# Kernel tuning notes

Measured on AMD Instinct MI355X. Metric: run time of the kernel, lower is better.

Reference implementation:

```python
import jax, jax.numpy as jnp
import numpy as np

B, T, H, NH, DH, R = 2, 2048, 1024, 16, 64, 256
ALPHA = 0.6


def setup_inputs() -> dict:
    key = jax.random.key(0)
    ks = jax.random.split(key, 28)
    f32 = jnp.float32

    def nrm(k, shape, s=0.02):
        return jax.random.normal(k, shape, dtype=f32) * s

    inp = {}
    inp['x'] = jax.random.normal(ks[0], (B, T, H), dtype=f32)
    # additive causal mask [1,1,T,T]: 0 on/below diagonal, -1e9 above
    causal = jnp.tril(jnp.ones((T, T), dtype=bool))
    inp['attention_mask'] = jnp.where(causal, 0.0, -1e9).astype(f32)[None, None]
    # low-rank SVD factors for q,k,v,o: Vh [H,R], S [R] (positive), U [H,R], b [H]
    i = 1
    for name in ('q', 'k', 'v', 'o'):
        inp['Vh_' + name] = nrm(ks[i], (H, R)); i += 1
        inp['S_' + name] = jax.random.uniform(ks[i], (R,), dtype=f32, minval=0.5, maxval=1.5); i += 1
        inp['U_' + name] = nrm(ks[i], (H, R)); i += 1
        inp['b_' + name] = jnp.zeros((H,), dtype=f32); i += 1
    # full-rank weights of the original (fallback) attention: y = x @ W + b (Conv1D style)
    for name in ('q', 'k', 'v', 'o'):
        inp['W_' + name] = nrm(ks[i], (H, H)); i += 1
        inp['bf_' + name] = jnp.zeros((H,), dtype=f32); i += 1
    return inp


def _split_heads(t):
    # [B,T,H] -> [B,nH,T,dH]
    Bs, Ts, _ = t.shape
    return t.reshape(Bs, Ts, NH, DH).transpose(0, 2, 1, 3)


def _attention(Q, K, V, mask):
    q, k, v = _split_heads(Q), _split_heads(K), _split_heads(V)
    scores = jnp.einsum('bhtd,bhsd->bhts', q, k) / (DH ** 0.5)
    scores = scores + mask
    w = jax.nn.softmax(scores, axis=-1)
    ctx = jnp.einsum('bhts,bhsd->bhtd', w, v)
    Bs = ctx.shape[0]
    return ctx.transpose(0, 2, 1, 3).reshape(Bs, -1, NH * DH)


def _lowrank(x, Vh, S, U, b):
    # ((x @ Vh) * S) @ U.T + b
    return ((x @ Vh) * S) @ U.T + b


def reference(x, attention_mask,
              Vh_q, S_q, U_q, b_q, Vh_k, S_k, U_k, b_k,
              Vh_v, S_v, U_v, b_v, Vh_o, S_o, U_o, b_o,
              W_q, bf_q, W_k, bf_k, W_v, bf_v, W_o, bf_o):
    # --- low-rank SVD path ---
    Q = _lowrank(x, Vh_q, S_q, U_q, b_q)
    K = _lowrank(x, Vh_k, S_k, U_k, b_k)
    V = _lowrank(x, Vh_v, S_v, U_v, b_v)
    ctx = _attention(Q, K, V, attention_mask)
    out = _lowrank(ctx, Vh_o, S_o, U_o, b_o)
    # --- fallback: original full-rank attention ---
    Qf = x @ W_q + bf_q
    Kf = x @ W_k + bf_k
    Vf = x @ W_v + bf_v
    ctxf = _attention(Qf, Kf, Vf, attention_mask)
    fallback_out = ctxf @ W_o + bf_o
    return ALPHA * out + (1.0 - ALPHA) * fallback_out
```

## Files before the change

### kernel.cpp

```cpp
#include <hip/hip_runtime.h>
#include <hip/hip_bf16.h>

typedef __bf16 bf16_t;
typedef __bf16 bf16x4 __attribute__((ext_vector_type(4)));
typedef __bf16 bf16x8 __attribute__((ext_vector_type(8)));
typedef float f32x4 __attribute__((ext_vector_type(4)));
typedef _Float16 f16_t;
typedef _Float16 f16x4 __attribute__((ext_vector_type(4)));
typedef unsigned short us4 __attribute__((ext_vector_type(4)));

extern "C" __device__ float __ocml_native_exp2_f32(float);

#define DEVI static __device__ __forceinline__

static constexpr int TN   = 2048;
static constexpr int Hn   = 1024;
static constexpr int Rn   = 256;
static constexpr int MTOK = 4096;
static constexpr int NCAT = 6144;

static constexpr float QSCALE = 0.125f;
static constexpr float LOG2E  = 1.44269504088896340736f;
static constexpr float SOFT_OFF2 = 0.426950408889634f;

template <typename T>
DEVI void gload16(const T* g, T* l) {
    __builtin_amdgcn_global_load_lds(
        (const __attribute__((address_space(1))) void*)g,
        (__attribute__((address_space(3))) void*)l, 16, 0, 0);
}

DEVI float loadf(const void* base, int idx, bool bfm) {
    if (bfm) {
        unsigned int u = ((const unsigned short*)base)[idx];
        u <<= 16;
        return __builtin_bit_cast(float, u);
    }
    return ((const float*)base)[idx];
}
DEVI float4 loadf4(const void* base, int idx, bool bfm) {
    float4 f;
    if (bfm) {
        us4 u = *(const us4*)((const unsigned short*)base + idx);
        f.x = __builtin_bit_cast(float, (unsigned)u.x << 16);
        f.y = __builtin_bit_cast(float, (unsigned)u.y << 16);
        f.z = __builtin_bit_cast(float, (unsigned)u.z << 16);
        f.w = __builtin_bit_cast(float, (unsigned)u.w << 16);
    } else {
        f = *(const float4*)((const float*)base + idx);
    }
    return f;
}
DEVI bool detect_bf16(const void* mask) {
    return fabsf(((const float*)mask)[0]) > 1.0f;
}

struct PrepArgs {
    const void *x, *mask;
    const void *Vh[4], *S[4], *U[4];
    const void *bb[4], *bfb[4];
    const void *W[4];
    bf16_t *wdst[4];
    int wldd[4];
    float wscale[4];
    bf16_t *Xb, *Abuf, *Bbuf, *Ubuf, *VhTs;
    float *biascat, *biaso;
};

__global__ __launch_bounds__(256)
void k_prep(PrepArgs a) {
    const bool bfm = detect_bf16(a.mask);
    const int bid = blockIdx.x;
    const int tid = threadIdx.x;
    __shared__ float t[32][33];
    if (bid < 1024) {
        int i = (bid * 256 + tid) * 16;
#pragma unroll
        for (int j = 0; j < 4; ++j) {
            float4 f = loadf4(a.x, i + j * 4, bfm);
            bf16x4 o;
            o[0] = (bf16_t)f.x; o[1] = (bf16_t)f.y; o[2] = (bf16_t)f.z; o[3] = (bf16_t)f.w;
            *(bf16x4*)&a.Xb[i + j * 4] = o;
        }
    } else if (bid < 1280) {
        int e4 = ((bid - 1024) * 256 + tid) * 4;
        int r = e4 & 255;
        float4 s4 = loadf4(a.S[3], r, bfm);
        float4 u4 = loadf4(a.U[3], e4, bfm);
        float4 v4 = loadf4(a.Vh[3], e4, bfm);
        bf16x4 ao, bo;
        ao[0] = (bf16_t)(u4.x * s4.x * 0.6f); ao[1] = (bf16_t)(u4.y * s4.y * 0.6f);
        ao[2] = (bf16_t)(u4.z * s4.z * 0.6f); ao[3] = (bf16_t)(u4.w * s4.w * 0.6f);
        bo[0] = (bf16_t)v4.x; bo[1] = (bf16_t)v4.y; bo[2] = (bf16_t)v4.z; bo[3] = (bf16_t)v4.w;
        *(bf16x4*)&a.Abuf[e4] = ao;
        *(bf16x4*)&a.Bbuf[e4] = bo;
    } else if (bid < 1472) {
        int i = ((bid - 1280) * 256 + tid) * 16;
        int proj = i >> 18;
        int e = i & 262143;
#pragma unroll
        for (int j = 0; j < 4; ++j) {
            float4 f = loadf4(a.U[proj], e + j * 4, bfm);
            bf16x4 o;
            o[0] = (bf16_t)f.x; o[1] = (bf16_t)f.y; o[2] = (bf16_t)f.z; o[3] = (bf16_t)f.w;
            *(bf16x4*)&a.Ubuf[i + j * 4] = o;
        }
    } else if (bid < 2240) {
        const int tb = bid - 1472;
        const int proj = tb >> 8;
        const int rem = tb & 255;
        const int bx = (rem & 7) * 32;
        const int by = (rem >> 3) * 32;
        const int tx = tid & 31, ty = tid >> 5;
        const float sc = (proj == 0) ? QSCALE * LOG2E : 1.0f;
        bf16_t* dst = a.VhTs + (size_t)proj * Rn * Hn;
#pragma unroll
        for (int k = 0; k < 32; k += 8)
            t[ty + k][tx] = loadf(a.Vh[proj], (by + ty + k) * Rn + bx + tx, bfm);
        __syncthreads();
#pragma unroll
        for (int k = 0; k < 32; k += 8) {
            const int r = bx + ty + k;
            dst[(size_t)r * Hn + by + tx] = (bf16_t)(sc * loadf(a.S[proj], r, bfm) * t[tx][ty + k]);
        }
    } else if (bid < 2268) {
        int i = (bid - 2240) * 256 + tid;
        if (i < 1024)      a.biascat[i] = QSCALE * LOG2E * loadf(a.bb[0], i, bfm);
        else if (i < 2048) a.biascat[i] = loadf(a.bb[1], i - 1024, bfm);
        else if (i < 3072) a.biascat[i] = loadf(a.bb[2], i - 2048, bfm);
        else if (i < 4096) a.biascat[i] = QSCALE * LOG2E * loadf(a.bfb[0], i - 3072, bfm);
        else if (i < 5120) a.biascat[i] = loadf(a.bfb[1], i - 4096, bfm);
        else if (i < 6144) a.biascat[i] = loadf(a.bfb[2], i - 5120, bfm);
        else {
            int j = i - 6144;
            a.biaso[j] = 0.6f * loadf(a.bb[3], j, bfm) + 0.4f * loadf(a.bfb[3], j, bfm);
        }
    } else {
        const int tb = bid - 2268;
        const int z  = tb >> 10;
        const int rem = tb & 1023;
        const int bx = (rem & 31) * 32, by = (rem >> 5) * 32;
        const int tx = tid & 31, ty = tid >> 5;
        const void* W = a.W[z];
        bf16_t* dst = a.wdst[z];
        const int ldd = a.wldd[z];
        const float scale = a.wscale[z];
#pragma unroll
        for (int k = 0; k < 32; k += 8)
            t[ty + k][tx] = loadf(W, (by + ty + k) * Hn + bx + tx, bfm);
        __syncthreads();
#pragma unroll
        for (int k = 0; k < 32; k += 8)
            dst[(size_t)(bx + ty + k) * ldd + by + tx] = (bf16_t)(scale * t[tx][ty + k]);
    }
}

template <int MI>
DEVI void gemm_core64(const bf16_t* __restrict__ A, int lda,
                      const bf16_t* __restrict__ B, int ldb, int K,
                      bf16_t* A0, bf16_t* A1, bf16_t* B0, bf16_t* B1,
                      int bm, int bn, f32x4 (&acc)[MI][4]) {
    constexpr int MT = MI * 32;
    const int tid  = threadIdx.x;
    const int lane = tid & 63;
    const int w    = tid >> 6;
    const int wr   = (w >> 1) * (MI * 16);
    const int wc   = (w & 1) * 64;
    const int fr   = lane & 15;
    const int quad = lane >> 4;

#pragma unroll
    for (int i = 0; i < MI; ++i)
#pragma unroll
        for (int j = 0; j < 4; ++j) acc[i][j] = {0.f, 0.f, 0.f, 0.f};

    for (int kb = 0; kb < K; kb += 64) {
        __syncthreads();
        for (int u = tid; u < MT * 4; u += 256) {
            const bf16_t* as = &A[(size_t)(bm + (u >> 2)) * lda + kb + (u & 3) * 8];
            gload16(as,      &A0[u * 8]);
            gload16(as + 32, &A1[u * 8]);
        }
#pragma unroll
        for (int t = 0; t < 2; ++t) {
            int u = t * 256 + tid;
            const bf16_t* bs = &B[(size_t)(bn + (u >> 2)) * ldb + kb + (u & 3) * 8];
            gload16(bs,      &B0[u * 8]);
            gload16(bs + 32, &B1[u * 8]);
        }
        __syncthreads();

#pragma unroll
        for (int kk = 0; kk < 2; ++kk) {
            const bf16_t* Ap = kk ? A1 : A0;
            const bf16_t* Bp = kk ? B1 : B0;
            bf16x8 af[MI], bfv[4];
#pragma unroll
            for (int i = 0; i < MI; ++i)
                af[i] = *(const bf16x8*)&Ap[(wr + i * 16 + fr) * 32 + quad * 8];
#pragma unroll
            for (int j = 0; j < 4; ++j)
                bfv[j] = *(const bf16x8*)&Bp[(wc + j * 16 + fr) * 32 + quad * 8];
#pragma unroll
            for (int i = 0; i < MI; ++i)
#pragma unroll
                for (int j = 0; j < 4; ++j)
                    acc[i][j] = __builtin_amdgcn_mfma_f32_16x16x32_bf16(af[i], bfv[j], acc[i][j], 0, 0, 0);
        }
    }
}

template <int MI, bool OUT_DUAL>
__global__ __launch_bounds__(256)
void k_gemm(const bf16_t* __restrict__ A, int lda,
            const bf16_t* __restrict__ B, int ldb,
            void* __restrict__ C, int ldc, int K,
            const float* __restrict__ bias, const void* __restrict__ mask) {
    constexpr int MT = MI * 32;
    __shared__ __align__(16) bf16_t A0[MT * 32], A1[MT * 32], B0[4096], B1[4096];

    const int tid  = threadIdx.x;
    const int lane = tid & 63;
    const int w    = tid >> 6;
    const int wr   = (w >> 1) * (MI * 16);
    const int wc   = (w & 1) * 64;
    const int bm   = blockIdx.x * MT;
    const int bn   = blockIdx.y * 128;
    const int fr   = lane & 15;
    const int quad = lane >> 4;

    f32x4 acc[MI][4];
    gemm_core64<MI>(A, lda, B, ldb, K, A0, A1, B0, B1, bm, bn, acc);

    bool bfm = false;
    if constexpr (OUT_DUAL) bfm = detect_bf16(mask);
#pragma unroll
    for (int i = 0; i < MI; ++i) {
        const int row0 = bm + wr + i * 16 + quad * 4;
#pragma unroll
        for (int j = 0; j < 4; ++j) {
            const int col = bn + wc + j * 16 + fr;
            const float bv = bias ? bias[col] : 0.f;
#pragma unroll
            for (int r = 0; r < 4; ++r) {
                float v = acc[i][j][r] + bv;
                size_t ci = (size_t)(row0 + r) * ldc + col;
                if constexpr (OUT_DUAL) {
                    if (bfm) ((unsigned short*)C)[ci] = __builtin_bit_cast(unsigned short, (bf16_t)v);
                    else     ((float*)C)[ci] = v;
                } else {
                    ((bf16_t*)C)[ci] = (bf16_t)v;
                }
            }
        }
    }
}

__global__ __launch_bounds__(256)
void k_small(const bf16_t* __restrict__ Abuf_o, const bf16_t* __restrict__ Bbuf_o,
             const bf16_t* __restrict__ Xb, const bf16_t* __restrict__ VhTs,
             bf16_t* __restrict__ Z, bf16_t* __restrict__ WoT) {
    __shared__ __align__(16) bf16_t A0[64 * 32], A1[64 * 32], B0[4096], B1[4096];
    const int x = blockIdx.x, y = blockIdx.y;

    const bf16_t* A; const bf16_t* B; bf16_t* C;
    int lda, ldb, ldc, K, bm, bn;
    if (y < 6) {
        A = Xb;   lda = Hn;  B = VhTs; ldb = Hn;  C = Z;   ldc = 768;  K = Hn;
        bm = x * 64; bn = y * 128;
    } else {
        A = Abuf_o; lda = Rn; B = Bbuf_o; ldb = Rn; C = WoT; ldc = 2048; K = Rn;
        bm = (x & 15) * 64; bn = ((y - 6) * 4 + (x >> 4)) * 128;
    }

    f32x4 acc[2][4];
    gemm_core64<2>(A, lda, B, ldb, K, A0, A1, B0, B1, bm, bn, acc);

    const int lane = threadIdx.x & 63;
    const int w    = threadIdx.x >> 6;
    const int wr   = (w >> 1) * 32;
    const int wc   = (w & 1) * 64;
    const int fr   = lane & 15;
    const int quad = lane >> 4;
#pragma unroll
    for (int i = 0; i < 2; ++i)
#pragma unroll
        for (int j = 0; j < 4; ++j)
#pragma unroll
            for (int r = 0; r < 4; ++r)
                C[(size_t)(bm + wr + i * 16 + quad * 4 + r) * ldc + bn + wc + j * 16 + fr]
                    = (bf16_t)acc[i][j][r];
}

__global__ __launch_bounds__(256)
void k_qkv(const bf16_t* __restrict__ Z, const bf16_t* __restrict__ Ubuf,
           const bf16_t* __restrict__ Xb, const bf16_t* __restrict__ Wfull,
           bf16_t* __restrict__ Yb, const float* __restrict__ bias,
           f16_t* __restrict__ Vt_g) {
    union SM { struct { bf16_t A0[128 * 32], A1[128 * 32], B0[4096], B1[4096]; } g;
               f16_t Ls[128 * 136]; };
    __shared__ __align__(16) SM sm;

    const int tid  = threadIdx.x;
    const int lane = tid & 63;
    const int w    = tid >> 6;
    const int wr   = (w >> 1) * 64;
    const int wc   = (w & 1) * 64;
    const int bm   = blockIdx.x * 128;
    const int fr   = lane & 15;
    const int quad = lane >> 4;

    const int yy   = blockIdx.y;
    const bool lrb = (yy & 1);
    const int half = yy >> 1;
    const int bn   = lrb ? half * 128 : 3072 + half * 128;

    const bf16_t* A; const bf16_t* B;
    int lda, ldb, K, bnb;
    if (lrb) {
        const int proj = bn >> 10;
        A = Z + proj * 256;  lda = 768;  K = 256;
        B = Ubuf + (size_t)proj * (Hn * Rn); ldb = Rn; bnb = bn & 1023;
    } else {
        A = Xb; lda = Hn; K = Hn;
        B = Wfull; ldb = Hn; bnb = bn - 3072;
    }

    f32x4 acc[4][4];
    gemm_core64<4>(A, lda, B, ldb, K, sm.g.A0, sm.g.A1, sm.g.B0, sm.g.B1, bm, bnb, acc);

    const bool isV = (bn >= 2048 && bn < 3072) || (bn >= 5120);
    if (isV) {
        const int pth = (bn >= 5120) ? 1 : 0;
        const int colrel = bn - (pth ? 5120 : 2048);
        const int bb = bm >> 11;
        const int R0 = (pth * 32 + bb * 16 + (colrel >> 6)) * 64;
        const int tloc = bm & 2047;
        __syncthreads();
#pragma unroll
        for (int i = 0; i < 4; ++i) {
            const int t0 = wr + i * 16 + quad * 4;
#pragma unroll
            for (int j = 0; j < 4; ++j) {
                const int c = wc + j * 16 + fr;
                const float bv = bias[bn + c];
#pragma unroll
                for (int r = 0; r < 4; ++r)
                    sm.Ls[c * 136 + t0 + r] = (f16_t)(acc[i][j][r] + bv);
            }
        }
        __syncthreads();
        const int c = tid >> 1, seg = tid & 1;
        f16_t* dst = &Vt_g[(size_t)(R0 + c) * TN + tloc + seg * 64];
        const f16_t* src = &sm.Ls[c * 136 + seg * 64];
#pragma unroll
        for (int e = 0; e < 8; ++e)
            *(uint4*)&dst[e * 8] = *(const uint4*)&src[e * 8];
        return;
    }

#pragma unroll
    for (int i = 0; i < 4; ++i) {
        const int row0 = bm + wr + i * 16 + quad * 4;
#pragma unroll
        for (int j = 0; j < 4; ++j) {
            const int col = bn + wc + j * 16 + fr;
            const float bv = bias[col];
#pragma unroll
            for (int r = 0; r < 4; ++r)
                Yb[(size_t)(row0 + r) * NCAT + col] = (bf16_t)(acc[i][j][r] + bv);
        }
    }
}

__global__ __launch_bounds__(256, 4)
void k_flash6(const bf16_t* __restrict__ Y, const f16_t* __restrict__ Vt_g,
              bf16_t* __restrict__ Ctx) {
    const int id   = blockIdx.x;
    const int inst = id & 63;
    const int slot = (id >> 6) & 3;
    const int rnd  = id >> 8;
    const int qt2  = (rnd == 0) ? 15 - slot
                   : (rnd == 1) ? 11 - slot
                   : (rnd == 2) ? 4 + slot
                                : slot;
    const int p = inst >> 5, b = (inst >> 4) & 1, h = inst & 15;

    const int tid  = threadIdx.x;
    const int lane = tid & 63;
    const int w    = tid >> 6;
    const int fr   = lane & 15;
    const int quad = lane >> 4;

    const int rowbase = b * TN;
    const int qbase   = qt2 * 128;
    const int qcol = p * 3072 + h * 64;
    const int kcol = qcol + 1024;
    const int ccol = p * 1024 + h * 64;

    __shared__ __align__(16) bf16_t Kb[2][2][64 * 32];
    __shared__ __align__(16) f16_t  Vb[2][64 * 64];

    const int r64 = tid >> 2;
    const int c8s = (((tid & 3) ^ ((tid >> 4) & 3)) * 8);
    const int ksw = (quad ^ ((fr >> 2) & 3)) * 8;

    size_t vsrc[2];
#pragma unroll
    for (int t = 0; t < 2; ++t) {
        int pp = w * 128 + t * 64 + lane;
        int d  = pp >> 3;
        vsrc[t] = (size_t)(inst * 64 + d) * TN + ((((pp & 7) - d) & 7) * 8);
    }

    f16x4 ones;
#pragma unroll
    for (int j = 0; j < 4; ++j) ones[j] = (f16_t)1.0f;

    const f32x4 off4 = {-SOFT_OFF2, -SOFT_OFF2, -SOFT_OFF2, -SOFT_OFF2};

    bf16x8 qf[2][2];
#pragma unroll
    for (int s = 0; s < 2; ++s) {
        const size_t qrow = (size_t)(rowbase + qbase + s * 64 + w * 16 + fr) * NCAT + qcol;
        qf[s][0] = *(const bf16x8*)&Y[qrow + quad * 8];
        qf[s][1] = *(const bf16x8*)&Y[qrow + 32 + quad * 8];
    }

    f32x4 o[2][4], lacc[2];
#pragma unroll
    for (int s = 0; s < 2; ++s) {
        lacc[s] = {0.f, 0.f, 0.f, 0.f};
#pragma unroll
        for (int db = 0; db < 4; ++db) o[s][db] = {0.f, 0.f, 0.f, 0.f};
    }

    const int t0 = (quad >> 1) + (fr & 7);
    const int h4 = (quad & 1) * 4;
    int voff[4];
#pragma unroll
    for (int nb = 0; nb < 4; ++nb) voff[nb] = ((nb * 2 + t0) & 7) * 8;

    const int kl = quad * 4;
    const int ql = w * 16 + fr;

    const int kmax = 2 * qt2 + 1;

    auto stage = [&](int kt, int bsel) {
        const bf16_t* ksrc = &Y[(size_t)(rowbase + kt * 64 + r64) * NCAT + kcol + c8s];
        gload16(ksrc,      &Kb[bsel][0][tid * 8]);
        gload16(ksrc + 32, &Kb[bsel][1][tid * 8]);
#pragma unroll
        for (int t = 0; t < 2; ++t)
            gload16(&Vt_g[vsrc[t] + kt * 64], &Vb[bsel][(w * 128 + t * 64 + lane) * 8]);
    };

    stage(0, 0);

    for (int kt = 0; kt <= kmax; ++kt) {
        const int cur = kt & 1;
        __syncthreads();
        if (kt < kmax) stage(kt + 1, cur ^ 1);

        const bool a0 = (kt < kmax);

        f16x4 pf[2][4];
#pragma unroll
        for (int nb = 0; nb < 4; ++nb) {
            const int ka = (nb * 16 + fr) * 32 + ksw;
            bf16x8 kf0 = *(const bf16x8*)&Kb[cur][0][ka];
            bf16x8 kf1 = *(const bf16x8*)&Kb[cur][1][ka];
#pragma unroll
            for (int s = 0; s < 2; ++s) {
                if (s == 0 && !a0) continue;
                f32x4 t4 = __builtin_amdgcn_mfma_f32_16x16x32_bf16(kf0, qf[s][0], off4, 0, 0, 0);
                t4 = __builtin_amdgcn_mfma_f32_16x16x32_bf16(kf1, qf[s][1], t4, 0, 0, 0);
                if (kt == 2 * qt2 + s) {
#pragma unroll
                    for (int r = 0; r < 4; ++r)
                        if (nb * 16 + kl + r > ql) t4[r] = -1e30f;
                }
                auto lo = __builtin_amdgcn_cvt_pkrtz(__ocml_native_exp2_f32(t4[0]),
                                                     __ocml_native_exp2_f32(t4[1]));
                auto hi = __builtin_amdgcn_cvt_pkrtz(__ocml_native_exp2_f32(t4[2]),
                                                     __ocml_native_exp2_f32(t4[3]));
                pf[s][nb] = __builtin_bit_cast(f16x4, __builtin_shufflevector(lo, hi, 0, 1, 2, 3));
            }
        }

#pragma unroll
        for (int s = 0; s < 2; ++s) {
            if (s == 0 && !a0) continue;
#pragma unroll
            for (int nb = 0; nb < 4; ++nb)
                lacc[s] = __builtin_amdgcn_mfma_f32_16x16x16f16(pf[s][nb], ones, lacc[s], 0, 0, 0);
        }

#pragma unroll
        for (int db = 0; db < 4; ++db) {
            const int vbase = (db * 16 + fr) * 64 + h4;
            f16x4 vf[4];
#pragma unroll
            for (int nb = 0; nb < 4; ++nb)
                vf[nb] = *(const f16x4*)&Vb[cur][vbase + voff[nb]];
#pragma unroll
            for (int nb = 0; nb < 4; ++nb) {
                o[1][db] = __builtin_amdgcn_mfma_f32_16x16x16f16(pf[1][nb], vf[nb], o[1][db], 0, 0, 0);
                if (a0)
                    o[0][db] = __builtin_amdgcn_mfma_f32_16x16x16f16(pf[0][nb], vf[nb], o[0][db], 0, 0, 0);
            }
        }
    }

#pragma unroll
    for (int s = 0; s < 2; ++s)
#pragma unroll
        for (int r = 0; r < 4; ++r) {
            const float inv = 1.0f / lacc[s][r];
            const size_t trow = (size_t)(rowbase + qbase + s * 64 + w * 16 + quad * 4 + r);
#pragma unroll
            for (int db = 0; db < 4; ++db)
                Ctx[trow * 2048 + ccol + db * 16 + fr] = (bf16_t)(o[s][db][r] * inv);
        }
}

extern "C" void kernel_launch(void* const* d_in, const int* in_sizes, int n_in,
                              void* d_out, int out_size, void* d_ws, size_t ws_size,
                              hipStream_t stream) {
    const void* x    = d_in[0];
    const void* mask = d_in[1];
    const void* Vh[4] = { d_in[2],  d_in[6],  d_in[10], d_in[14] };
    const void* Sp[4] = { d_in[3],  d_in[7],  d_in[11], d_in[15] };
    const void* Up[4] = { d_in[4],  d_in[8],  d_in[12], d_in[16] };
    const void* bb[4] = { d_in[5],  d_in[9],  d_in[13], d_in[17] };
    const void* Wp[4] = { d_in[18], d_in[20], d_in[22], d_in[24] };
    const void* bf[4] = { d_in[19], d_in[21], d_in[23], d_in[25] };

    char* ws = (char*)d_ws;
    size_t off = 0;
    auto alloc = [&](size_t bytes) -> void* {
        void* p = ws + off;
        off = (off + bytes + 255) & ~(size_t)255;
        return p;
    };
    bf16_t* Xb      = (bf16_t*)alloc((size_t)MTOK * Hn * 2);
    bf16_t* Wfull   = (bf16_t*)alloc((size_t)3 * Hn * Hn * 2);
    bf16_t* Yb      = (bf16_t*)alloc((size_t)MTOK * NCAT * 2);
    bf16_t* Ctx     = (bf16_t*)alloc((size_t)MTOK * 2048 * 2);
    bf16_t* WoT     = (bf16_t*)alloc((size_t)Hn * 2048 * 2);
    f16_t*  Vt_g    = (f16_t*)alloc((size_t)64 * 64 * TN * 2);
    bf16_t* Zbuf    = (bf16_t*)alloc((size_t)MTOK * 768 * 2);
    bf16_t* Ubuf    = (bf16_t*)alloc((size_t)3 * Hn * Rn * 2);
    bf16_t* VhTs    = (bf16_t*)alloc((size_t)3 * Rn * Hn * 2);
    bf16_t* Abuf    = (bf16_t*)alloc((size_t)Hn * Rn * 2);
    bf16_t* Bbuf    = (bf16_t*)alloc((size_t)Hn * Rn * 2);
    float*  biascat = (float*)alloc(NCAT * 4);
    float*  biaso   = (float*)alloc(Hn * 4);

    PrepArgs pa;
    pa.x = x; pa.mask = mask;
    for (int i = 0; i < 4; ++i) {
        pa.Vh[i] = Vh[i]; pa.S[i] = Sp[i]; pa.U[i] = Up[i];
        pa.bb[i] = bb[i]; pa.bfb[i] = bf[i];
        pa.W[i] = Wp[i];
    }
    for (int i = 0; i < 3; ++i) {
        pa.wdst[i] = Wfull + (size_t)i * Hn * Hn;
        pa.wldd[i] = Hn;
        pa.wscale[i] = (i == 0) ? QSCALE * LOG2E : 1.0f;
    }
    pa.wdst[3] = WoT + 1024; pa.wldd[3] = 2048; pa.wscale[3] = 0.4f;
    pa.Xb = Xb; pa.Abuf = Abuf; pa.Bbuf = Bbuf; pa.Ubuf = Ubuf; pa.VhTs = VhTs;
    pa.biascat = biascat; pa.biaso = biaso;
    k_prep<<<6364, 256, 0, stream>>>(pa);

    k_small<<<dim3(64, 8), 256, 0, stream>>>(Abuf, Bbuf, Xb, VhTs, Zbuf, WoT);

    k_qkv<<<dim3(32, 48), 256, 0, stream>>>(
        Zbuf, Ubuf, Xb, Wfull, Yb, biascat, Vt_g);

    k_flash6<<<1024, 256, 0, stream>>>(Yb, Vt_g, Ctx);

    k_gemm<4, true><<<dim3(32, 8), 256, 0, stream>>>(
        Ctx, 2048, WoT, 2048, d_out, Hn, 2048, biaso, mask);
}
```

Baseline: 300.5 us.

## Use fp16 for low-rank intermediates, enlarge k_small tiles, raise flash occupancy

```diff
diff --git a/kernel.cpp b/kernel.cpp
--- a/kernel.cpp
+++ b/kernel.cpp
@@ -7,6 +7,7 @@
 typedef float f32x4 __attribute__((ext_vector_type(4)));
 typedef _Float16 f16_t;
 typedef _Float16 f16x4 __attribute__((ext_vector_type(4)));
+typedef _Float16 f16x8 __attribute__((ext_vector_type(8)));
 typedef unsigned short us4 __attribute__((ext_vector_type(4)));
 
 extern "C" __device__ float __ocml_native_exp2_f32(float);
@@ -63,7 +64,8 @@
     bf16_t *wdst[4];
     int wldd[4];
     float wscale[4];
-    bf16_t *Xb, *Abuf, *Bbuf, *Ubuf, *VhTs;
+    bf16_t *Xb, *Abuf, *Bbuf, *VhTs;
+    f16_t *Ubuf;
     float *biascat, *biaso;
 };
 
@@ -101,9 +103,9 @@
 #pragma unroll
         for (int j = 0; j < 4; ++j) {
             float4 f = loadf4(a.U[proj], e + j * 4, bfm);
-            bf16x4 o;
-            o[0] = (bf16_t)f.x; o[1] = (bf16_t)f.y; o[2] = (bf16_t)f.z; o[3] = (bf16_t)f.w;
-            *(bf16x4*)&a.Ubuf[i + j * 4] = o;
+            f16x4 o;
+            o[0] = (f16_t)f.x; o[1] = (f16_t)f.y; o[2] = (f16_t)f.z; o[3] = (f16_t)f.w;
+            *(f16x4*)&a.Ubuf[i + j * 4] = o;
         }
     } else if (bid < 2240) {
         const int tb = bid - 1472;
@@ -155,7 +157,7 @@
     }
 }
 
-template <int MI>
+template <int MI, bool HALF = false>
 DEVI void gemm_core64(const bf16_t* __restrict__ A, int lda,
                       const bf16_t* __restrict__ B, int ldb, int K,
                       bf16_t* A0, bf16_t* A1, bf16_t* B0, bf16_t* B1,
@@ -204,8 +206,15 @@
 #pragma unroll
             for (int i = 0; i < MI; ++i)
 #pragma unroll
-                for (int j = 0; j < 4; ++j)
-                    acc[i][j] = __builtin_amdgcn_mfma_f32_16x16x32_bf16(af[i], bfv[j], acc[i][j], 0, 0, 0);
+                for (int j = 0; j < 4; ++j) {
+                    if constexpr (HALF)
+                        acc[i][j] = __builtin_amdgcn_mfma_f32_16x16x32_f16(
+                            __builtin_bit_cast(f16x8, af[i]),
+                            __builtin_bit_cast(f16x8, bfv[j]), acc[i][j], 0, 0, 0);
+                    else
+                        acc[i][j] = __builtin_amdgcn_mfma_f32_16x16x32_bf16(
+                            af[i], bfv[j], acc[i][j], 0, 0, 0);
+                }
         }
     }
 }
@@ -259,41 +268,46 @@
 __global__ __launch_bounds__(256)
 void k_small(const bf16_t* __restrict__ Abuf_o, const bf16_t* __restrict__ Bbuf_o,
              const bf16_t* __restrict__ Xb, const bf16_t* __restrict__ VhTs,
-             bf16_t* __restrict__ Z, bf16_t* __restrict__ WoT) {
-    __shared__ __align__(16) bf16_t A0[64 * 32], A1[64 * 32], B0[4096], B1[4096];
+             f16_t* __restrict__ Z, bf16_t* __restrict__ WoT) {
+    __shared__ __align__(16) bf16_t A0[128 * 32], A1[128 * 32], B0[4096], B1[4096];
     const int x = blockIdx.x, y = blockIdx.y;
-
-    const bf16_t* A; const bf16_t* B; bf16_t* C;
-    int lda, ldb, ldc, K, bm, bn;
-    if (y < 6) {
-        A = Xb;   lda = Hn;  B = VhTs; ldb = Hn;  C = Z;   ldc = 768;  K = Hn;
-        bm = x * 64; bn = y * 128;
-    } else {
-        A = Abuf_o; lda = Rn; B = Bbuf_o; ldb = Rn; C = WoT; ldc = 2048; K = Rn;
-        bm = (x & 15) * 64; bn = ((y - 6) * 4 + (x >> 4)) * 128;
-    }
-
-    f32x4 acc[2][4];
-    gemm_core64<2>(A, lda, B, ldb, K, A0, A1, B0, B1, bm, bn, acc);
 
     const int lane = threadIdx.x & 63;
     const int w    = threadIdx.x >> 6;
-    const int wr   = (w >> 1) * 32;
+    const int wr   = (w >> 1) * 64;
     const int wc   = (w & 1) * 64;
     const int fr   = lane & 15;
     const int quad = lane >> 4;
-#pragma unroll
-    for (int i = 0; i < 2; ++i)
-#pragma unroll
-        for (int j = 0; j < 4; ++j)
-#pragma unroll
-            for (int r = 0; r < 4; ++r)
-                C[(size_t)(bm + wr + i * 16 + quad * 4 + r) * ldc + bn + wc + j * 16 + fr]
-                    = (bf16_t)acc[i][j][r];
+
+    f32x4 acc[4][4];
+    if (y < 6) {
+        const int bm = x * 128, bn = y * 128;
+        gemm_core64<4>(Xb, Hn, VhTs, Hn, Hn, A0, A1, B0, B1, bm, bn, acc);
+#pragma unroll
+        for (int i = 0; i < 4; ++i)
+#pragma unroll
+            for (int j = 0; j < 4; ++j)
+#pragma unroll
+                for (int r = 0; r < 4; ++r)
+                    Z[(size_t)(bm + wr + i * 16 + quad * 4 + r) * 768 + bn + wc + j * 16 + fr]
+                        = (f16_t)acc[i][j][r];
+    } else {
+        const int idx = (y - 6) * 32 + x;
+        const int bm = (idx & 7) * 128, bn = (idx >> 3) * 128;
+        gemm_core64<4>(Abuf_o, Rn, Bbuf_o, Rn, Rn, A0, A1, B0, B1, bm, bn, acc);
+#pragma unroll
+        for (int i = 0; i < 4; ++i)
+#pragma unroll
+            for (int j = 0; j < 4; ++j)
+#pragma unroll
+                for (int r = 0; r < 4; ++r)
+                    WoT[(size_t)(bm + wr + i * 16 + quad * 4 + r) * 2048 + bn + wc + j * 16 + fr]
+                        = (bf16_t)acc[i][j][r];
+    }
 }
 
 __global__ __launch_bounds__(256)
-void k_qkv(const bf16_t* __restrict__ Z, const bf16_t* __restrict__ Ubuf,
+void k_qkv(const f16_t* __restrict__ Z, const f16_t* __restrict__ Ubuf,
            const bf16_t* __restrict__ Xb, const bf16_t* __restrict__ Wfull,
            bf16_t* __restrict__ Yb, const float* __restrict__ bias,
            f16_t* __restrict__ Vt_g) {
@@ -315,19 +329,16 @@
     const int half = yy >> 1;
     const int bn   = lrb ? half * 128 : 3072 + half * 128;
 
-    const bf16_t* A; const bf16_t* B;
-    int lda, ldb, K, bnb;
+    f32x4 acc[4][4];
     if (lrb) {
         const int proj = bn >> 10;
-        A = Z + proj * 256;  lda = 768;  K = 256;
-        B = Ubuf + (size_t)proj * (Hn * Rn); ldb = Rn; bnb = bn & 1023;
+        gemm_core64<4, true>((const bf16_t*)(Z + proj * 256), 768,
+                             (const bf16_t*)(Ubuf + (size_t)proj * (Hn * Rn)), Rn, 256,
+                             sm.g.A0, sm.g.A1, sm.g.B0, sm.g.B1, bm, bn & 1023, acc);
     } else {
-        A = Xb; lda = Hn; K = Hn;
-        B = Wfull; ldb = Hn; bnb = bn - 3072;
-    }
-
-    f32x4 acc[4][4];
-    gemm_core64<4>(A, lda, B, ldb, K, sm.g.A0, sm.g.A1, sm.g.B0, sm.g.B1, bm, bnb, acc);
+        gemm_core64<4, false>(Xb, Hn, Wfull, Hn, Hn,
+                              sm.g.A0, sm.g.A1, sm.g.B0, sm.g.B1, bm, bn - 3072, acc);
+    }
 
     const bool isV = (bn >= 2048 && bn < 3072) || (bn >= 5120);
     if (isV) {
@@ -373,7 +384,7 @@
     }
 }
 
-__global__ __launch_bounds__(256, 4)
+__global__ __launch_bounds__(256, 5)
 void k_flash6(const bf16_t* __restrict__ Y, const f16_t* __restrict__ Vt_g,
               bf16_t* __restrict__ Ctx) {
     const int id   = blockIdx.x;
@@ -549,8 +560,8 @@
     bf16_t* Ctx     = (bf16_t*)alloc((size_t)MTOK * 2048 * 2);
     bf16_t* WoT     = (bf16_t*)alloc((size_t)Hn * 2048 * 2);
     f16_t*  Vt_g    = (f16_t*)alloc((size_t)64 * 64 * TN * 2);
-    bf16_t* Zbuf    = (bf16_t*)alloc((size_t)MTOK * 768 * 2);
-    bf16_t* Ubuf    = (bf16_t*)alloc((size_t)3 * Hn * Rn * 2);
+    f16_t*  Zbuf    = (f16_t*)alloc((size_t)MTOK * 768 * 2);
+    f16_t*  Ubuf    = (f16_t*)alloc((size_t)3 * Hn * Rn * 2);
     bf16_t* VhTs    = (bf16_t*)alloc((size_t)3 * Rn * Hn * 2);
     bf16_t* Abuf    = (bf16_t*)alloc((size_t)Hn * Rn * 2);
     bf16_t* Bbuf    = (bf16_t*)alloc((size_t)Hn * Rn * 2);
@@ -574,7 +585,7 @@
     pa.biascat = biascat; pa.biaso = biaso;
     k_prep<<<6364, 256, 0, stream>>>(pa);
 
-    k_small<<<dim3(64, 8), 256, 0, stream>>>(Abuf, Bbuf, Xb, VhTs, Zbuf, WoT);
+    k_small<<<dim3(32, 8), 256, 0, stream>>>(Abuf, Bbuf, Xb, VhTs, Zbuf, WoT);
 
     k_qkv<<<dim3(32, 48), 256, 0, stream>>>(
         Zbuf, Ubuf, Xb, Wfull, Yb, biascat, Vt_g);
```

New measurement: 380.8 us. +26.7%, slower.
